# Kernel optimization log

Hardware: AMD Instinct MI355X
Metric: run time of the kernel (lower is better)

## Reference

```python
import math
import jax, jax.numpy as jnp
import numpy as np

D_MODEL, N_STATE, SEQ_LEN = 1024, 64, 1024
DT_MIN, DT_MAX = 1e-3, 1e-1


def setup_inputs() -> dict:
    key = jax.random.key(0)
    kC, kdt = jax.random.split(key)
    A_real = -0.5 * jnp.ones((D_MODEL, N_STATE), jnp.float32)
    A_imag = math.pi * jnp.broadcast_to(
        jnp.arange(N_STATE, dtype=jnp.float32), (D_MODEL, N_STATE)
    )
    C = jax.random.normal(kC, (D_MODEL, N_STATE, 2), jnp.float32) * 0.5
    log_dt = (
        jax.random.uniform(kdt, (D_MODEL,), jnp.float32)
        * (math.log(DT_MAX) - math.log(DT_MIN))
        + math.log(DT_MIN)
    )
    B = jnp.ones((D_MODEL, N_STATE), jnp.float32)
    return {"A_real": A_real, "A_imag": A_imag, "C": C, "log_dt": log_dt,
            "B": B, "L": SEQ_LEN}


def reference(A_real, A_imag, C, log_dt, B, L):
    dt = jnp.exp(log_dt)                       # (d,)
    A = A_real + 1j * A_imag                   # (d,N) complex64
    dtA = A * dt[:, None]                      # (d,N)
    Cc = C[..., 0] + 1j * C[..., 1]            # (d,N) complex64
    ell = jnp.arange(L, dtype=jnp.float32)     # (L,)
    # A_bar ** l == exp(dtA * l): Vandermonde power expansion, (d,N,L)
    powers = jnp.exp(dtA[..., None] * ell)
    K = jnp.einsum('dn,dnl->dl', Cc * B.astype(Cc.dtype), powers)  # (d,L)
    return K.real * dt[:, None]
```

## Files before the change

### kernel.cpp

```cpp
#include <hip/hip_runtime.h>
#include <math.h>


#define D_MODEL 1024
#define N_STATE 64
#define SEQ_LEN 1024
#define CHUNK   8
#define TPD     (SEQ_LEN / CHUNK)
#define DPB     2
#define BLOCK   (TPD * DPB)

#define INV_2PI 0.15915494309189535

__device__ __forceinline__ float sin_rev(float f) { return __builtin_amdgcn_sinf(f); }
__device__ __forceinline__ float cos_rev(float f) { return __builtin_amdgcn_cosf(f); }

__global__ __launch_bounds__(BLOCK) void s4d_kernel(
    const float* __restrict__ A_real, const float* __restrict__ A_imag,
    const float* __restrict__ C, const float* __restrict__ log_dt,
    const float* __restrict__ B, float* __restrict__ out)
{
  __shared__ float4 sA[DPB][N_STATE];
  __shared__ float4 sB[DPB][N_STATE];

  const int tid = threadIdx.x;

  if (tid < DPB * N_STATE) {
    const int ld = tid >> 6;
    const int n  = tid & (N_STATE - 1);
    const int d  = blockIdx.x * DPB + ld;
    const float dt = __expf(log_dt[d]);
    const float ar = A_real[d * N_STATE + n];
    const float ai = A_imag[d * N_STATE + n];
    const float b  = B[d * N_STATE + n];
    const float cr = C[(d * N_STATE + n) * 2 + 0];
    const float ci = C[(d * N_STATE + n) * 2 + 1];

    const float xr = dt * ar;
    const double drev = (double)dt * (double)ai * INV_2PI;
    const float hi = (float)drev;
    const float lo = (float)(drev - (double)hi);

    const float  eS = __expf(xr * (float)TPD);
    const double rS = drev * (double)TPD;
    const float  fS = (float)(rS - floor(rS));
    const float str = eS * cos_rev(fS);
    const float sti = eS * sin_rev(fS);

    sA[ld][n] = make_float4(xr, cr * b * dt, ci * b * dt, str);
    sB[ld][n] = make_float4(sti, hi, lo, 0.0f);
  }
  __syncthreads();

  const int ld = tid / TPD;
  const int t  = tid % TPD;
  const int d  = blockIdx.x * DPB + ld;
  const float tf = (float)t;

  float acc[CHUNK];
  #pragma unroll
  for (int j = 0; j < CHUNK; ++j) acc[j] = 0.0f;

  #pragma unroll 2
  for (int n = 0; n < N_STATE; ++n) {
    const float4 a  = sA[ld][n];
    const float4 bv = sB[ld][n];
    const float xr = a.x, wr = a.y, wi = a.z, str = a.w;
    const float sti = bv.x, hi = bv.y, lo = bv.z;

    float p = tf * hi;
    float e = fmaf(tf, hi, -p);
    float f = (p - floorf(p)) + fmaf(tf, lo, e);
    f -= floorf(f);

    const float c0 = cos_rev(f);
    const float s0 = sin_rev(f);
    const float e0 = __expf(xr * tf);

    float yr = e0 * fmaf(wr, c0, -(wi * s0));
    float yi = e0 * fmaf(wr, s0,   wi * c0);

    #pragma unroll
    for (int j = 0; j < CHUNK; ++j) {
      acc[j] += yr;
      const float nyr = fmaf(yr, str, -(yi * sti));
      yi = fmaf(yr, sti, yi * str);
      yr = nyr;
    }
  }

  float* op = out + d * SEQ_LEN + t;
  #pragma unroll
  for (int j = 0; j < CHUNK; ++j) op[j * TPD] = acc[j];
}

extern "C" void kernel_launch(void* const* d_in, const int* in_sizes, int n_in,
                              void* d_out, int out_size, void* d_ws, size_t ws_size,
                              hipStream_t stream) {
  const float* A_real = (const float*)d_in[0];
  const float* A_imag = (const float*)d_in[1];
  const float* C      = (const float*)d_in[2];
  const float* log_dt = (const float*)d_in[3];
  const float* B      = (const float*)d_in[4];
  float* out = (float*)d_out;

  dim3 grid(D_MODEL / DPB);
  dim3 block(BLOCK);
  s4d_kernel<<<grid, block, 0, stream>>>(A_real, A_imag, C, log_dt, B, out);
}
```

Before: 78.97 us.

## Replace per-thread transcendentals with factored power tables and real recurrence

Removes the per-thread sin/cos/exp evaluation in the state loop. Each block now precomputes per-state tables of A_bar^(16*hi) and A_bar^lo in shared memory, and each thread forms its starting power with one complex multiply. The eight outputs per state then come from a second-order real recurrence (u_{k+2} = 2Re(s)u_{k+1} - |s|^2 u_k) instead of a full complex rotation. The state dimension is split across two thread halves and combined through a shared-memory reduction, with one d_model row per block. This adds table setup work, a second barrier and a reduction, and the product of two float table entries may carry slightly different rounding than direct evaluation.

```diff
diff --git a/kernel.cpp b/kernel.cpp
--- a/kernel.cpp
+++ b/kernel.cpp
@@ -6,92 +6,106 @@
 #define N_STATE 64
 #define SEQ_LEN 1024
 #define CHUNK   8
-#define TPD     (SEQ_LEN / CHUNK)
-#define DPB     2
-#define BLOCK   (TPD * DPB)
+#define TPD     128
+#define NSPLIT  2
+#define NPT     (N_STATE / NSPLIT)
+#define BLOCK   (TPD * NSPLIT)
 
 #define INV_2PI 0.15915494309189535
 
 __device__ __forceinline__ float sin_rev(float f) { return __builtin_amdgcn_sinf(f); }
 __device__ __forceinline__ float cos_rev(float f) { return __builtin_amdgcn_cosf(f); }
 
-__global__ __launch_bounds__(BLOCK) void s4d_kernel(
+__global__ __launch_bounds__(BLOCK, 4) void s4d_kernel(
     const float* __restrict__ A_real, const float* __restrict__ A_imag,
     const float* __restrict__ C, const float* __restrict__ log_dt,
     const float* __restrict__ B, float* __restrict__ out)
 {
-  __shared__ float4 sA[DPB][N_STATE];
-  __shared__ float4 sB[DPB][N_STATE];
+  __shared__ float2 hiT[N_STATE][8];
+  __shared__ float2 loT[N_STATE][16];
+  __shared__ float4 ws[N_STATE];
+  __shared__ float  red[CHUNK][TPD];
 
   const int tid = threadIdx.x;
+  const int d   = blockIdx.x;
+  const float dt = __expf(log_dt[d]);
 
-  if (tid < DPB * N_STATE) {
-    const int ld = tid >> 6;
-    const int n  = tid & (N_STATE - 1);
-    const int d  = blockIdx.x * DPB + ld;
-    const float dt = __expf(log_dt[d]);
+  #pragma unroll
+  for (int i = 0; i < 6; ++i) {
+    const int e   = tid + BLOCK * i;
+    const int n   = e / 24;
+    const int idx = e - n * 24;
+    const int steps = (idx < 8) ? (idx << 4) : (idx - 8);
+    const float ar = A_real[d * N_STATE + n];
+    const float ai = A_imag[d * N_STATE + n];
+    const float xr = dt * ar;
+    const double drev = (double)dt * (double)ai * INV_2PI;
+    const double ph = drev * (double)steps;
+    const float  fr = (float)(ph - floor(ph));
+    const float mag = __expf(xr * (float)steps);
+    const float2 v = make_float2(mag * cos_rev(fr), mag * sin_rev(fr));
+    if (idx < 8) hiT[n][idx] = v; else loT[n][idx - 8] = v;
+  }
+  if (tid < N_STATE) {
+    const int n = tid;
     const float ar = A_real[d * N_STATE + n];
     const float ai = A_imag[d * N_STATE + n];
     const float b  = B[d * N_STATE + n];
     const float cr = C[(d * N_STATE + n) * 2 + 0];
     const float ci = C[(d * N_STATE + n) * 2 + 1];
-
     const float xr = dt * ar;
     const double drev = (double)dt * (double)ai * INV_2PI;
-    const float hi = (float)drev;
-    const float lo = (float)(drev - (double)hi);
-
-    const float  eS = __expf(xr * (float)TPD);
-    const double rS = drev * (double)TPD;
-    const float  fS = (float)(rS - floor(rS));
-    const float str = eS * cos_rev(fS);
-    const float sti = eS * sin_rev(fS);
-
-    sA[ld][n] = make_float4(xr, cr * b * dt, ci * b * dt, str);
-    sB[ld][n] = make_float4(sti, hi, lo, 0.0f);
+    const double ph = drev * 128.0;
+    const float  fr = (float)(ph - floor(ph));
+    const float mag = __expf(xr * 128.0f);
+    ws[n] = make_float4(cr * b * dt, ci * b * dt,
+                        mag * cos_rev(fr), mag * sin_rev(fr));
   }
   __syncthreads();
 
-  const int ld = tid / TPD;
-  const int t  = tid % TPD;
-  const int d  = blockIdx.x * DPB + ld;
-  const float tf = (float)t;
+  const int t     = tid & (TPD - 1);
+  const int split = tid >> 7;
+  const int thi   = t >> 4;
+  const int tlo   = t & 15;
 
   float acc[CHUNK];
   #pragma unroll
   for (int j = 0; j < CHUNK; ++j) acc[j] = 0.0f;
 
-  #pragma unroll 2
-  for (int n = 0; n < N_STATE; ++n) {
-    const float4 a  = sA[ld][n];
-    const float4 bv = sB[ld][n];
-    const float xr = a.x, wr = a.y, wi = a.z, str = a.w;
-    const float sti = bv.x, hi = bv.y, lo = bv.z;
-
-    float p = tf * hi;
-    float e = fmaf(tf, hi, -p);
-    float f = (p - floorf(p)) + fmaf(tf, lo, e);
-    f -= floorf(f);
-
-    const float c0 = cos_rev(f);
-    const float s0 = sin_rev(f);
-    const float e0 = __expf(xr * tf);
-
-    float yr = e0 * fmaf(wr, c0, -(wi * s0));
-    float yi = e0 * fmaf(wr, s0,   wi * c0);
-
+  const int n0 = split * NPT;
+  #pragma unroll 4
+  for (int nn = 0; nn < NPT; ++nn) {
+    const int n = n0 + nn;
+    const float4 w4 = ws[n];
+    const float2 h  = hiT[n][thi];
+    const float2 l2 = loT[n][tlo];
+    const float sr = fmaf(h.x, l2.x, -(h.y * l2.y));
+    const float si = fmaf(h.x, l2.y,   h.y * l2.x);
+    float u0 = fmaf(w4.x, sr, -(w4.y * si));
+    const float yi = fmaf(w4.x, si, w4.y * sr);
+    float u1 = fmaf(u0, w4.z, -(yi * w4.w));
+    const float a2 = w4.z + w4.z;
+    const float nb = -fmaf(w4.z, w4.z, w4.w * w4.w);
+    acc[0] += u0;
+    acc[1] += u1;
     #pragma unroll
-    for (int j = 0; j < CHUNK; ++j) {
-      acc[j] += yr;
-      const float nyr = fmaf(yr, str, -(yi * sti));
-      yi = fmaf(yr, sti, yi * str);
-      yr = nyr;
+    for (int j = 2; j < CHUNK; ++j) {
+      const float u2 = fmaf(a2, u1, nb * u0);
+      acc[j] += u2;
+      u0 = u1; u1 = u2;
     }
   }
 
-  float* op = out + d * SEQ_LEN + t;
-  #pragma unroll
-  for (int j = 0; j < CHUNK; ++j) op[j * TPD] = acc[j];
+  if (split == 1) {
+    #pragma unroll
+    for (int j = 0; j < CHUNK; ++j) red[j][t] = acc[j];
+  }
+  __syncthreads();
+  if (split == 0) {
+    float* op = out + d * SEQ_LEN + t;
+    #pragma unroll
+    for (int j = 0; j < CHUNK; ++j) op[j * TPD] = acc[j] + red[j][t];
+  }
 }
 
 extern "C" void kernel_launch(void* const* d_in, const int* in_sizes, int n_in,
@@ -104,7 +118,6 @@
   const float* B      = (const float*)d_in[4];
   float* out = (float*)d_out;
 
-  dim3 grid(D_MODEL / DPB);
-  dim3 block(BLOCK);
-  s4d_kernel<<<grid, block, 0, stream>>>(A_real, A_imag, C, log_dt, B, out);
+  s4d_kernel<<<dim3(D_MODEL), dim3(BLOCK), 0, stream>>>(
+      A_real, A_imag, C, log_dt, B, out);
 }
```

After: 72.36 us. 8.4% less time.
